# Kernel optimization log

Hardware: AMD Instinct MI355X
Metric: run time of the kernel (lower is better)

The kernel has to match this reference:

```python
import jax, jax.numpy as jnp
import numpy as np

N_FFT = 256
HOP = 64
HS = 126  # window hop in STFT frames (hard-coded in original)


def _stft(x):
    # torch.stft(center=True, pad_mode='reflect', window=None -> rectangular,
    # onesided=True, normalized=False). x: [B, N] -> [B, T, F] (time-major,
    # matching the module's permute(0,1,3,2)).
    pad = N_FFT // 2
    xp = jnp.pad(x, ((0, 0), (pad, pad)), mode='reflect')
    T = x.shape[-1] // HOP + 1
    idx = jnp.arange(T)[:, None] * HOP + jnp.arange(N_FFT)[None, :]  # [T, n_fft]
    frames = xp[:, idx]  # [B, T, n_fft]
    return jnp.fft.rfft(frames, axis=-1)  # [B, T, F=129]


def _spec_match(mix, aux):
    mixS = _stft(mix[:, 0, :])  # [B, Tm, F] complex
    auxS = _stft(aux[:, 0, :])  # [B, Ta, F] complex
    B, Tm, F = mixS.shape
    Ta = auxS.shape[1]
    length = (Ta - Tm) // HS
    pad = HS - (Ta - Tm) % HS
    auxS = jnp.pad(auxS, ((0, 0), (0, pad), (0, 0)))
    # All sliding windows at once: [B, W, Tm, F]
    W = length + 2
    widx = jnp.arange(W)[:, None] * HS + jnp.arange(Tm)[None, :]  # [W, Tm]
    wins = auxS[:, widx, :]  # [B, W, Tm, F]
    # Real part of complex cosine similarity, elementwise
    m = mixS[:, None]  # [B, 1, Tm, F]
    sim = (m.real * wins.real + m.imag * wins.imag) / (jnp.abs(m) * jnp.abs(wins))
    flat = sim.reshape(B, W, -1)
    n = flat.shape[-1]
    # torch.median = lower median; torch.median returns NaN if any NaN present
    srt = jnp.sort(flat, axis=-1)
    med = srt[..., (n - 1) // 2]
    med = jnp.where(jnp.isnan(flat).any(-1), -jnp.inf, med)
    best = jnp.argmax(med, axis=1)  # [B], first max like Python max()
    sel = jnp.take_along_axis(wins, best[:, None, None, None], axis=1)  # [B,1,Tm,F]
    return jnp.concatenate([sel.real, sel.imag], axis=1)  # [B, 2, Tm, F]


def setup_inputs() -> dict:
    key = jax.random.key(0)
    k1, k2 = jax.random.split(key)
    mix = jax.random.normal(k1, (8, 1, 65536), dtype=jnp.float32)
    aux = jax.random.normal(k2, (8, 1, 262144), dtype=jnp.float32)
    return {"mix": mix, "aux": aux}


def reference(mix, aux):
    return _spec_match(mix, aux)
```

## Files before the change

### kernel.cpp

```cpp
#include <hip/hip_runtime.h>
#include <math.h>

constexpr int NFFT  = 256;
constexpr int HOP   = 64;
constexpr int NBIN  = 129;
constexpr int NB    = 8;
constexpr int LMIX  = 65536;
constexpr int LAUX  = 262144;
constexpr int TM    = 1025;
constexpr int TA    = 4097;
constexpr int TROWS = 4175;
constexpr int HS    = 126;
constexpr int W     = 26;
constexpr int NJOBS = NB * W;
constexpr int NVAL  = TM * NBIN;
constexpr int KMED  = (NVAL - 1) / 2;
constexpr int CHUNKS = 8;
constexpr int NBA   = 1024;
constexpr int FPB   = 4;
constexpr int MIXBLKS = (TM + FPB - 1) / FPB;
constexpr int AUXBLKS = (TROWS + FPB - 1) / FPB;
constexpr int GFPB  = 4;
constexpr int GBLKS = (TM + GFPB - 1) / GFPB;

constexpr size_t MIXN_OFF  = 0;
constexpr size_t MIXN_BYTES = (size_t)NB * TM * NBIN * sizeof(float2);
constexpr size_t AUXN_OFF  = MIXN_OFF + MIXN_BYTES;
constexpr size_t AUXN_BYTES = (size_t)NB * TROWS * NBIN * sizeof(float2);
constexpr size_t HIST_OFF  = AUXN_OFF + AUXN_BYTES;
constexpr size_t HIST_BYTES = (size_t)NJOBS * CHUNKS * NBA * 4;
constexpr size_t CAND_OFF  = HIST_OFF + HIST_BYTES;
constexpr size_t CAND_BYTES = (size_t)NJOBS * NVAL * 4;
constexpr size_t NAN_OFF   = CAND_OFF + CAND_BYTES;
constexpr size_t NAN_BYTES = (size_t)NJOBS * CHUNKS * 4;
constexpr size_t NCAND_OFF = NAN_OFF + NAN_BYTES;
constexpr size_t KREM_OFF  = NCAND_OFF + 832;
constexpr size_t MED_OFF   = KREM_OFF + 832;

constexpr float TWOPI_N = (float)(-2.0 * 3.14159265358979323846 / 256.0);

__device__ __forceinline__ float2 twiddle(int k) {
    float s, c;
    sincosf(TWOPI_N * (float)k, &s, &c);
    return make_float2(c, s);
}

__global__ void stft_all(const float* __restrict__ mix, const float* __restrict__ aux,
                         float2* __restrict__ mixN, float2* __restrict__ auxN,
                         unsigned* __restrict__ ncand)
{
    constexpr int NX = 64 * (FPB - 1) + NFFT;
    __shared__ float  xs[NX];
    __shared__ float2 Yl[FPB][16][16];
    __shared__ float2 cis16[16];

    const int tid  = threadIdx.x;
    const int wgid = blockIdx.x;
    const int b    = wgid & 7;
    const int t    = wgid >> 3;
    const bool isMix = t < MIXBLKS;
    const int f0 = (isMix ? t : t - MIXBLKS) * FPB;
    const int L       = isMix ? LMIX : LAUX;
    const int Tframes = isMix ? TM : TA;
    const int Trows   = isMix ? TM : TROWS;
    const float* x    = isMix ? mix : aux;
    float2* out       = isMix ? mixN : auxN;

    if (wgid == 0 && tid < NJOBS) ncand[tid] = 0u;

    if (tid < 16) cis16[tid] = twiddle(16 * tid);

    for (int i = tid; i < NX; i += 256) {
        int j = f0 * HOP + i - 128;
        if (j < 0) j = -j;
        if (j >= L) j = 2 * L - 2 - j;
        xs[i] = x[(size_t)b * L + j];
    }
    __syncthreads();

    const int n1 = (tid >> 4) & 15;
    const int r  = tid & 15;
    {
        float reA[FPB], imA[FPB];
        #pragma unroll
        for (int f = 0; f < FPB; ++f) { reA[f] = 0.f; imA[f] = 0.f; }
        int idx = 0;
        #pragma unroll
        for (int n2 = 0; n2 < 16; ++n2) {
            float2 tv = cis16[idx];
            #pragma unroll
            for (int f = 0; f < FPB; ++f) {
                float v = xs[f * HOP + n1 + 16 * n2];
                reA[f] = fmaf(v, tv.x, reA[f]);
                imA[f] = fmaf(v, tv.y, imA[f]);
            }
            idx = (idx + r) & 15;
        }
        #pragma unroll
        for (int f = 0; f < FPB; ++f) Yl[f][n1][r] = make_float2(reA[f], imA[f]);
    }
    __syncthreads();

    const float QNAN = __int_as_float(0x7FC00000);
    auto emit = [&](int fr, int k, float ar, float ai) {
        if (fr >= Trows) return;
        float2 o;
        if (fr < Tframes) {
            float inv = rsqrtf(ar * ar + ai * ai);
            o = make_float2(ar * inv, ai * inv);
        } else {
            o = make_float2(QNAN, QNAN);
        }
        out[((size_t)b * Trows + fr) * NBIN + k] = o;
    };

    {
        const int jjA = tid, jjB = tid + 256;
        const int fA = jjA / NBIN, kA = jjA - fA * NBIN;
        const int fB = jjB / NBIN, kB = jjB - fB * NBIN;
        const float2 dkA = twiddle(kA);
        const float2 dkB = twiddle(kB);
        float trA = 1.f, tiA = 0.f, arA = 0.f, aiA = 0.f;
        float trB = 1.f, tiB = 0.f, arB = 0.f, aiB = 0.f;
        #pragma unroll
        for (int s = 0; s < 16; ++s) {
            float2 yA = Yl[fA][s][kA & 15];
            float2 yB = Yl[fB][s][kB & 15];
            arA = fmaf(trA, yA.x, arA); arA = fmaf(-tiA, yA.y, arA);
            aiA = fmaf(trA, yA.y, aiA); aiA = fmaf( tiA, yA.x, aiA);
            arB = fmaf(trB, yB.x, arB); arB = fmaf(-tiB, yB.y, arB);
            aiB = fmaf(trB, yB.y, aiB); aiB = fmaf( tiB, yB.x, aiB);
            float nrA = trA * dkA.x - tiA * dkA.y;
            tiA = fmaf(trA, dkA.y, tiA * dkA.x); trA = nrA;
            float nrB = trB * dkB.x - tiB * dkB.y;
            tiB = fmaf(trB, dkB.y, tiB * dkB.x); trB = nrB;
        }
        emit(f0 + fA, kA, arA, aiA);
        emit(f0 + fB, kB, arB, aiB);
    }
    if (tid < FPB * NBIN - 512) {
        const int jj = 512 + tid;
        const int f = jj / NBIN, k = jj - f * NBIN;
        const float2 dk = twiddle(k);
        float tr = 1.f, ti = 0.f, ar = 0.f, ai = 0.f;
        #pragma unroll
        for (int s = 0; s < 16; ++s) {
            float2 y = Yl[f][s][k & 15];
            ar = fmaf(tr, y.x, ar); ar = fmaf(-ti, y.y, ar);
            ai = fmaf(tr, y.y, ai); ai = fmaf( ti, y.x, ai);
            float nr = tr * dk.x - ti * dk.y;
            ti = fmaf(tr, dk.y, ti * dk.x); tr = nr;
        }
        emit(f0 + f, k, ar, ai);
    }
}

__device__ __forceinline__ unsigned flip_key(float s) {
    unsigned u = __float_as_uint(s);
    return (u & 0x80000000u) ? ~u : (u | 0x80000000u);
}
__device__ __forceinline__ unsigned qbin(float s) {
    if (!(s == s)) return (unsigned)(NBA - 1);
    int bq = (int)floorf(fmaf(s, 512.f, 512.f));
    bq = max(0, min(NBA - 1, bq));
    return (unsigned)bq;
}

template<int PER>
__device__ __forceinline__ void rank_find(const unsigned (&bins)[PER], unsigned target,
                                          unsigned& out_bin, unsigned& out_rem)
{
    __shared__ unsigned wtot[4];
    __shared__ unsigned result[2];
    const int tid  = threadIdx.x;
    const int lane = tid & 63;
    const int wid  = tid >> 6;

    unsigned st = 0;
    #pragma unroll
    for (int i = 0; i < PER; ++i) st += bins[i];

    unsigned inc = st;
    #pragma unroll
    for (int d = 1; d < 64; d <<= 1) {
        unsigned v = __shfl_up(inc, d);
        if (lane >= d) inc += v;
    }
    if (lane == 63) wtot[wid] = inc;
    __syncthreads();

    unsigned wbase = 0;
    for (int wme = 0; wme < wid; ++wme) wbase += wtot[wme];
    unsigned ex = wbase + inc - st;
    if ((ex <= target) && (target < ex + st)) {
        unsigned cum = ex;
        #pragma unroll
        for (int i = 0; i < PER; ++i) {
            if (cum + bins[i] > target) {
                result[0] = (unsigned)(tid * PER + i);
                result[1] = target - cum;
                break;
            }
            cum += bins[i];
        }
    }
    __syncthreads();
    out_bin = result[0];
    out_rem = result[1];
}

__global__ void sim_hist(const float2* __restrict__ mixN, const float2* __restrict__ auxN,
                         unsigned* __restrict__ hist, unsigned* __restrict__ nanCnt)
{
    constexpr int NCOPY   = 4;
    constexpr int HSTRIDE = NBA + 1;
    __shared__ unsigned lh[NCOPY * HSTRIDE];
    __shared__ unsigned bnan;
    const int tid   = threadIdx.x;
    const int wgid  = blockIdx.x;
    const int b     = wgid & 7;
    const int rest  = wgid >> 3;
    const int w     = rest / CHUNKS;
    const int chunk = rest - w * CHUNKS;
    const int job   = b * W + w;
    unsigned* lhc = lh + ((tid >> 4) & (NCOPY - 1)) * HSTRIDE;

    for (int i = tid; i < NCOPY * HSTRIDE; i += 256) lh[i] = 0;
    if (tid == 0) bnan = 0;
    __syncthreads();

    unsigned localnan = 0;
    const float2* mrow = mixN + (size_t)b * TM * NBIN;
    const float2* arow = auxN + ((size_t)b * TROWS + (size_t)w * HS) * NBIN;

    const int pad = b & 1;
    const int lim = pad + ((NVAL - pad) & ~1);

    for (int i = pad + (chunk * 256 + tid) * 2; i < lim; i += CHUNKS * 512) {
        float4 mv = *reinterpret_cast<const float4*>(mrow + i);
        float4 av = *reinterpret_cast<const float4*>(arow + i);
        float s0 = fmaf(mv.x, av.x, mv.y * av.y);
        float s1 = fmaf(mv.z, av.z, mv.w * av.w);
        if (!(s0 == s0)) localnan++;
        if (!(s1 == s1)) localnan++;
        atomicAdd(&lhc[qbin(s0)], 1u);
        atomicAdd(&lhc[qbin(s1)], 1u);
    }
    if (chunk == 0 && tid == 0) {
        int ie = pad ? 0 : NVAL - 1;
        float2 m = mrow[ie];
        float2 a = arow[ie];
        float s = fmaf(m.x, a.x, m.y * a.y);
        if (!(s == s)) localnan++;
        atomicAdd(&lhc[qbin(s)], 1u);
    }
    if (localnan) atomicAdd(&bnan, localnan);
    __syncthreads();

    unsigned* gh = hist + ((size_t)job * CHUNKS + chunk) * NBA;
    for (int i = tid; i < NBA; i += 256)
        gh[i] = lh[i] + lh[HSTRIDE + i] + lh[2 * HSTRIDE + i] + lh[3 * HSTRIDE + i];
    if (tid == 0) nanCnt[job * CHUNKS + chunk] = bnan;
}

__global__ void sim_compact(const float2* __restrict__ mixN, const float2* __restrict__ auxN,
                            const unsigned* __restrict__ hist, unsigned* __restrict__ cand,
                            unsigned* __restrict__ ncand, unsigned* __restrict__ krem)
{
    const int tid   = threadIdx.x;
    const int wgid  = blockIdx.x;
    const int b     = wgid & 7;
    const int rest  = wgid >> 3;
    const int w     = rest / CHUNKS;
    const int chunk = rest - w * CHUNKS;
    const int job   = b * W + w;

    unsigned bins[NBA / 256];
    const unsigned* h = hist + (size_t)job * CHUNKS * NBA;
    #pragma unroll
    for (int i = 0; i < NBA / 256; ++i) {
        unsigned v = 0;
        int bin = tid * (NBA / 256) + i;
        #pragma unroll
        for (int c = 0; c < CHUNKS; ++c) v += h[(size_t)c * NBA + bin];
        bins[i] = v;
    }
    unsigned sb, rem;
    rank_find<NBA / 256>(bins, (unsigned)KMED, sb, rem);
    if (chunk == 0 && tid == 0) krem[job] = rem;

    unsigned* candj  = cand + (size_t)job * NVAL;
    unsigned* ncandj = ncand + job;
    const int lane = tid & 63;

    const float2* mrow = mixN + (size_t)b * TM * NBIN;
    const float2* arow = auxN + ((size_t)b * TROWS + (size_t)w * HS) * NBIN;

    const int pad = b & 1;
    const int lim = pad + ((NVAL - pad) & ~1);

    for (int i = pad + (chunk * 256 + tid) * 2; i < lim; i += CHUNKS * 512) {
        float4 mv = *reinterpret_cast<const float4*>(mrow + i);
        float4 av = *reinterpret_cast<const float4*>(arow + i);
        float sv[2];
        sv[0] = fmaf(mv.x, av.x, mv.y * av.y);
        sv[1] = fmaf(mv.z, av.z, mv.w * av.w);
        #pragma unroll
        for (int u = 0; u < 2; ++u) {
            bool pred = (qbin(sv[u]) == sb);
            unsigned long long m = __ballot(pred);
            if (m) {
                int leader = __ffsll(m) - 1;
                unsigned base = 0;
                if (lane == leader) base = atomicAdd(ncandj, (unsigned)__popcll(m));
                base = (unsigned)__shfl((int)base, leader);
                if (pred) candj[base + __popcll(m & ((1ull << lane) - 1ull))] = flip_key(sv[u]);
            }
        }
    }
    if (chunk == 0 && tid == 0) {
        int ie = pad ? 0 : NVAL - 1;
        float2 m = mrow[ie];
        float2 a = arow[ie];
        float s = fmaf(m.x, a.x, m.y * a.y);
        if (qbin(s) == sb) {
            unsigned idx = atomicAdd(ncandj, 1u);
            candj[idx] = flip_key(s);
        }
    }
}

__global__ void select_kernel(const unsigned* __restrict__ cand, const unsigned* __restrict__ ncand,
                              const unsigned* __restrict__ krem, const unsigned* __restrict__ nanCnt,
                              float* __restrict__ med)
{
    __shared__ unsigned h[2048];
    const int wgid = blockIdx.x;
    const int job  = (wgid & 7) * W + (wgid >> 3);
    const int tid  = threadIdx.x;
    const unsigned* c = cand + (size_t)job * NVAL;
    const unsigned n = ncand[job];
    unsigned pref = 0, tgt = krem[job];

    for (int ph = 0; ph < 3; ++ph) {
        for (int i = tid; i < 2048; i += 256) h[i] = 0;
        __syncthreads();
        for (unsigned i = tid; i < n; i += 256) {
            unsigned k = c[i];
            if (ph == 0) atomicAdd(&h[k >> 21], 1u);
            else if (ph == 1) { if ((k >> 21) == (pref >> 21)) atomicAdd(&h[(k >> 10) & 2047u], 1u); }
            else { if ((k >> 10) == (pref >> 10)) atomicAdd(&h[k & 1023u], 1u); }
        }
        __syncthreads();

        unsigned bins[8];
        #pragma unroll
        for (int i = 0; i < 8; ++i) bins[i] = h[tid * 8 + i];
        unsigned sb, rem;
        rank_find<8>(bins, tgt, sb, rem);

        if (ph == 0)      pref = sb << 21;
        else if (ph == 1) pref |= sb << 10;
        else              pref |= sb;
        tgt = rem;
        __syncthreads();
    }

    if (tid == 0) {
        unsigned nan = 0;
        #pragma unroll
        for (int c2 = 0; c2 < CHUNKS; ++c2) nan += nanCnt[job * CHUNKS + c2];
        unsigned key = pref;
        unsigned u = (key & 0x80000000u) ? (key ^ 0x80000000u) : ~key;
        med[job] = (nan > 0u) ? -INFINITY : __uint_as_float(u);
    }
}

__global__ void gather_stft(const float* __restrict__ x, const float* __restrict__ med,
                            float* __restrict__ out)
{
    constexpr int NX = 64 * (GFPB - 1) + NFFT;
    __shared__ float  xs[NX];
    __shared__ float2 Yl[GFPB][16][16];
    __shared__ float2 cis16[16];
    __shared__ int sh_best;

    const int tid  = threadIdx.x;
    const int wgid = blockIdx.x;
    const int b    = wgid & 7;
    const int t0   = (wgid >> 3) * GFPB;

    if (tid == 0) {
        float mx = -INFINITY; int bi = 0;
        for (int w = 0; w < W; ++w) {
            float v = med[b * W + w];
            if (v > mx) { mx = v; bi = w; }
        }
        sh_best = bi;
    }
    if (tid < 16) cis16[tid] = twiddle(16 * tid);
    __syncthreads();

    const int fr0 = sh_best * HS + t0;

    for (int i = tid; i < NX; i += 256) {
        int j = fr0 * HOP + i - 128;
        if (j < 0) j = -j;
        if (j >= LAUX) j = 2 * LAUX - 2 - j;
        j = max(0, min(LAUX - 1, j));
        xs[i] = x[(size_t)b * LAUX + j];
    }
    __syncthreads();

    const int n1 = (tid >> 4) & 15;
    const int r  = tid & 15;
    {
        float reA[GFPB], imA[GFPB];
        #pragma unroll
        for (int f = 0; f < GFPB; ++f) { reA[f] = 0.f; imA[f] = 0.f; }
        int idx = 0;
        #pragma unroll
        for (int n2 = 0; n2 < 16; ++n2) {
            float2 tv = cis16[idx];
            #pragma unroll
            for (int f = 0; f < GFPB; ++f) {
                float v = xs[f * HOP + n1 + 16 * n2];
                reA[f] = fmaf(v, tv.x, reA[f]);
                imA[f] = fmaf(v, tv.y, imA[f]);
            }
            idx = (idx + r) & 15;
        }
        #pragma unroll
        for (int f = 0; f < GFPB; ++f) Yl[f][n1][r] = make_float2(reA[f], imA[f]);
    }
    __syncthreads();

    auto dotask = [&](int jj) {
        const int f = jj / NBIN, k = jj - f * NBIN;
        const int tt = t0 + f;
        if (tt >= TM) return;
        float ar = 0.f, ai = 0.f;
        if (fr0 + f < TA) {
            const float2 dk = twiddle(k);
            float tr = 1.f, ti = 0.f;
            #pragma unroll
            for (int s = 0; s < 16; ++s) {
                float2 y = Yl[f][s][k & 15];
                ar = fmaf(tr, y.x, ar); ar = fmaf(-ti, y.y, ar);
                ai = fmaf(tr, y.y, ai); ai = fmaf( ti, y.x, ai);
                float nr = tr * dk.x - ti * dk.y;
                ti = fmaf(tr, dk.y, ti * dk.x); tr = nr;
            }
        }
        size_t o = (size_t)tt * NBIN + k;
        out[(size_t)(b * 2 + 0) * NVAL + o] = ar;
        out[(size_t)(b * 2 + 1) * NVAL + o] = ai;
    };
    dotask(tid);
    dotask(tid + 256);
    if (tid < GFPB * NBIN - 512) dotask(512 + tid);
}

extern "C" void kernel_launch(void* const* d_in, const int* in_sizes, int n_in,
                              void* d_out, int out_size, void* d_ws, size_t ws_size,
                              hipStream_t stream)
{
    const float* mix = (const float*)d_in[0];
    const float* aux = (const float*)d_in[1];
    float* out = (float*)d_out;
    char* ws = (char*)d_ws;

    float2*   mixN = (float2*)(ws + MIXN_OFF);
    float2*   auxN = (float2*)(ws + AUXN_OFF);
    unsigned* hist = (unsigned*)(ws + HIST_OFF);
    unsigned* cand = (unsigned*)(ws + CAND_OFF);
    unsigned* nanC = (unsigned*)(ws + NAN_OFF);
    unsigned* ncand= (unsigned*)(ws + NCAND_OFF);
    unsigned* krem = (unsigned*)(ws + KREM_OFF);
    float*    med  = (float*)(ws + MED_OFF);

    stft_all<<<(MIXBLKS + AUXBLKS) * NB, 256, 0, stream>>>(mix, aux, mixN, auxN, ncand);
    sim_hist<<<NJOBS * CHUNKS, 256, 0, stream>>>(mixN, auxN, hist, nanC);
    sim_compact<<<NJOBS * CHUNKS, 256, 0, stream>>>(mixN, auxN, hist, cand, ncand, krem);
    select_kernel<<<NJOBS, 256, 0, stream>>>(cand, ncand, krem, nanC, med);
    gather_stft<<<GBLKS * NB, 256, 0, stream>>>(aux, med, out);
}
```

Measured before the change: 118.9 us.

## Split histogram rank scan into own kernel, cache twiddles in LDS, double frames per block

Moves the per-job histogram reduction and rank search out of sim_compact into a new scan_bins kernel, so each job runs it once instead of once in every chunk block. Precomputes a 256-entry twiddle table in shared memory so per-bin sincosf calls become LDS reads in the STFT and gather kernels. Raises STFT frames per block from 4 to 8, with a loop over two passes, to cut block count and redundant setup. This costs an extra kernel launch and more shared memory per STFT block.

```diff
diff --git a/kernel.cpp b/kernel.cpp
--- a/kernel.cpp
+++ b/kernel.cpp
@@ -17,7 +17,7 @@
 constexpr int KMED  = (NVAL - 1) / 2;
 constexpr int CHUNKS = 8;
 constexpr int NBA   = 1024;
-constexpr int FPB   = 4;
+constexpr int FPB   = 8;
 constexpr int MIXBLKS = (TM + FPB - 1) / FPB;
 constexpr int AUXBLKS = (TROWS + FPB - 1) / FPB;
 constexpr int GFPB  = 4;
@@ -34,7 +34,8 @@
 constexpr size_t NAN_OFF   = CAND_OFF + CAND_BYTES;
 constexpr size_t NAN_BYTES = (size_t)NJOBS * CHUNKS * 4;
 constexpr size_t NCAND_OFF = NAN_OFF + NAN_BYTES;
-constexpr size_t KREM_OFF  = NCAND_OFF + 832;
+constexpr size_t SELBIN_OFF= NCAND_OFF + 832;
+constexpr size_t KREM_OFF  = SELBIN_OFF + 832;
 constexpr size_t MED_OFF   = KREM_OFF + 832;
 
 constexpr float TWOPI_N = (float)(-2.0 * 3.14159265358979323846 / 256.0);
@@ -52,6 +53,7 @@
     constexpr int NX = 64 * (FPB - 1) + NFFT;
     __shared__ float  xs[NX];
     __shared__ float2 Yl[FPB][16][16];
+    __shared__ float2 tw256[256];
     __shared__ float2 cis16[16];
 
     const int tid  = threadIdx.x;
@@ -68,6 +70,7 @@
 
     if (wgid == 0 && tid < NJOBS) ncand[tid] = 0u;
 
+    tw256[tid] = twiddle(tid);
     if (tid < 16) cis16[tid] = twiddle(16 * tid);
 
     for (int i = tid; i < NX; i += 256) {
@@ -114,12 +117,14 @@
         out[((size_t)b * Trows + fr) * NBIN + k] = o;
     };
 
-    {
-        const int jjA = tid, jjB = tid + 256;
+    #pragma unroll 1
+    for (int p = 0; p < 2; ++p) {
+        const int jjA = tid + 512 * p;
+        const int jjB = jjA + 256;
         const int fA = jjA / NBIN, kA = jjA - fA * NBIN;
         const int fB = jjB / NBIN, kB = jjB - fB * NBIN;
-        const float2 dkA = twiddle(kA);
-        const float2 dkB = twiddle(kB);
+        const float2 dkA = tw256[kA];
+        const float2 dkB = tw256[kB];
         float trA = 1.f, tiA = 0.f, arA = 0.f, aiA = 0.f;
         float trB = 1.f, tiB = 0.f, arB = 0.f, aiB = 0.f;
         #pragma unroll
@@ -138,10 +143,10 @@
         emit(f0 + fA, kA, arA, aiA);
         emit(f0 + fB, kB, arB, aiB);
     }
-    if (tid < FPB * NBIN - 512) {
-        const int jj = 512 + tid;
+    if (tid < FPB * NBIN - 1024) {
+        const int jj = 1024 + tid;
         const int f = jj / NBIN, k = jj - f * NBIN;
-        const float2 dk = twiddle(k);
+        const float2 dk = tw256[k];
         float tr = 1.f, ti = 0.f, ar = 0.f, ai = 0.f;
         #pragma unroll
         for (int s = 0; s < 16; ++s) {
@@ -263,9 +268,32 @@
     if (tid == 0) nanCnt[job * CHUNKS + chunk] = bnan;
 }
 
+__global__ void scan_bins(const unsigned* __restrict__ hist, unsigned* __restrict__ selbin,
+                          unsigned* __restrict__ krem)
+{
+    constexpr int PER = NBA / 256;
+    const int tid  = threadIdx.x;
+    const int wgid = blockIdx.x;
+    const int job  = (wgid & 7) * W + (wgid >> 3);
+    const unsigned* h = hist + (size_t)job * CHUNKS * NBA;
+
+    unsigned bins[PER];
+    #pragma unroll
+    for (int i = 0; i < PER; ++i) {
+        unsigned v = 0;
+        int bin = tid * PER + i;
+        #pragma unroll
+        for (int c = 0; c < CHUNKS; ++c) v += h[(size_t)c * NBA + bin];
+        bins[i] = v;
+    }
+    unsigned sb, rem;
+    rank_find<PER>(bins, (unsigned)KMED, sb, rem);
+    if (tid == 0) { selbin[job] = sb; krem[job] = rem; }
+}
+
 __global__ void sim_compact(const float2* __restrict__ mixN, const float2* __restrict__ auxN,
-                            const unsigned* __restrict__ hist, unsigned* __restrict__ cand,
-                            unsigned* __restrict__ ncand, unsigned* __restrict__ krem)
+                            const unsigned* __restrict__ selbin, unsigned* __restrict__ cand,
+                            unsigned* __restrict__ ncand)
 {
     const int tid   = threadIdx.x;
     const int wgid  = blockIdx.x;
@@ -274,20 +302,7 @@
     const int w     = rest / CHUNKS;
     const int chunk = rest - w * CHUNKS;
     const int job   = b * W + w;
-
-    unsigned bins[NBA / 256];
-    const unsigned* h = hist + (size_t)job * CHUNKS * NBA;
-    #pragma unroll
-    for (int i = 0; i < NBA / 256; ++i) {
-        unsigned v = 0;
-        int bin = tid * (NBA / 256) + i;
-        #pragma unroll
-        for (int c = 0; c < CHUNKS; ++c) v += h[(size_t)c * NBA + bin];
-        bins[i] = v;
-    }
-    unsigned sb, rem;
-    rank_find<NBA / 256>(bins, (unsigned)KMED, sb, rem);
-    if (chunk == 0 && tid == 0) krem[job] = rem;
+    const unsigned sb = selbin[job];
 
     unsigned* candj  = cand + (size_t)job * NVAL;
     unsigned* ncandj = ncand + job;
@@ -382,6 +397,7 @@
     constexpr int NX = 64 * (GFPB - 1) + NFFT;
     __shared__ float  xs[NX];
     __shared__ float2 Yl[GFPB][16][16];
+    __shared__ float2 tw256[256];
     __shared__ float2 cis16[16];
     __shared__ int sh_best;
 
@@ -398,6 +414,7 @@
         }
         sh_best = bi;
     }
+    tw256[tid] = twiddle(tid);
     if (tid < 16) cis16[tid] = twiddle(16 * tid);
     __syncthreads();
 
@@ -441,7 +458,7 @@
         if (tt >= TM) return;
         float ar = 0.f, ai = 0.f;
         if (fr0 + f < TA) {
-            const float2 dk = twiddle(k);
+            const float2 dk = tw256[k];
             float tr = 1.f, ti = 0.f;
             #pragma unroll
             for (int s = 0; s < 16; ++s) {
@@ -476,12 +493,14 @@
     unsigned* cand = (unsigned*)(ws + CAND_OFF);
     unsigned* nanC = (unsigned*)(ws + NAN_OFF);
     unsigned* ncand= (unsigned*)(ws + NCAND_OFF);
+    unsigned* selb = (unsigned*)(ws + SELBIN_OFF);
     unsigned* krem = (unsigned*)(ws + KREM_OFF);
     float*    med  = (float*)(ws + MED_OFF);
 
     stft_all<<<(MIXBLKS + AUXBLKS) * NB, 256, 0, stream>>>(mix, aux, mixN, auxN, ncand);
     sim_hist<<<NJOBS * CHUNKS, 256, 0, stream>>>(mixN, auxN, hist, nanC);
-    sim_compact<<<NJOBS * CHUNKS, 256, 0, stream>>>(mixN, auxN, hist, cand, ncand, krem);
+    scan_bins<<<NJOBS, 256, 0, stream>>>(hist, selb, krem);
+    sim_compact<<<NJOBS * CHUNKS, 256, 0, stream>>>(mixN, auxN, selb, cand, ncand);
     select_kernel<<<NJOBS, 256, 0, stream>>>(cand, ncand, krem, nanC, med);
     gather_stft<<<GBLKS * NB, 256, 0, stream>>>(aux, med, out);
 }
```

Result: slower. 122.9 us (+3.3%).
